# Kernel tuning notes

Measured on AMD Instinct MI355X. Metric: run time of the kernel, lower is better.

Reference implementation:

```python
import jax, jax.numpy as jnp
import numpy as np

M_TOKENS, D_IN, D_OUT = 4096, 4096, 16384


def setup_inputs() -> dict:
    key = jax.random.key(0)
    k1, k2, k3, k4 = jax.random.split(key, 4)
    x = jax.random.normal(k1, (M_TOKENS, D_IN), dtype=jnp.float32)
    # pre-quantized int8 weight, stored [K, N] as in qweight_kn
    qweight_kn = jax.random.randint(k2, (D_IN, D_OUT), -127, 128, dtype=jnp.int8)
    # per-output-channel weight dequant scales (float16 buffer, used as fp32 in kernel)
    weight_scales = jax.random.uniform(k3, (D_OUT,), dtype=jnp.float32, minval=1e-3, maxval=2e-2)
    bias = jax.random.normal(k4, (D_OUT,), dtype=jnp.float32) * 0.01
    return {"x": x, "qweight_kn": qweight_kn, "weight_scales": weight_scales, "bias": bias}


def reference(x, qweight_kn, weight_scales, bias):
    target_dtype = x.dtype
    x2 = x.reshape(-1, x.shape[-1])  # [M, K]
    # dynamic per-token (per-row) symmetric quantization
    x_max = jnp.max(jnp.abs(x2), axis=-1, keepdims=True).astype(jnp.float32) + 1e-5
    x_scales = x_max / 127.0  # [M, 1]
    x_int8 = jnp.clip(jnp.round(x2.astype(jnp.float32) / x_scales), -128, 127).astype(jnp.int8)
    acc = jax.lax.dot_general(
        x_int8, qweight_kn,
        dimension_numbers=(((1,), (0,)), ((), ())),
        preferred_element_type=jnp.int32,
    )  # [M, N] int32
    # fused dequant: row act-scale * col weight-scale, plus bias
    c = acc.astype(jnp.float32) * x_scales * weight_scales[None, :].astype(jnp.float32)
    c = c + bias[None, :]
    out = c.astype(jnp.bfloat16)  # kernel stores bf16
    return out.reshape(*x.shape[:-1], -1).astype(target_dtype)
```

## Files before the change

### kernel.cpp

```cpp
#include <hip/hip_runtime.h>
#include <hip/hip_bf16.h>
#include <stdint.h>

typedef int v4i __attribute__((ext_vector_type(4)));

#define GM 4096
#define GN 16384
#define GK 4096
#define BM 256
#define BN 256
#define BK 64
#define NT (GK / BK)

__device__ __forceinline__ void gload16(const void* g, void* l) {
  __builtin_amdgcn_global_load_lds(
      (const __attribute__((address_space(1))) void*)g,
      (__attribute__((address_space(3))) void*)l, 16, 0, 0);
}

__global__ __launch_bounds__(256) void quant_rows(
    const float* __restrict__ x, int8_t* __restrict__ xq2,
    float* __restrict__ xs, int K) {
  const int row = blockIdx.x;
  const int t = threadIdx.x;
  const float4* src = (const float4*)(x + (size_t)row * K) + t * 4;
  float4 v[4];
  float m = 0.f;
#pragma unroll
  for (int i = 0; i < 4; ++i) {
    v[i] = src[i];
    m = fmaxf(m, fmaxf(fmaxf(fabsf(v[i].x), fabsf(v[i].y)),
                       fmaxf(fabsf(v[i].z), fabsf(v[i].w))));
  }
#pragma unroll
  for (int off = 1; off < 64; off <<= 1)
    m = fmaxf(m, __shfl_xor(m, off, 64));
  __shared__ float wmax[4];
  if ((t & 63) == 0) wmax[t >> 6] = m;
  __syncthreads();
  const float gm = fmaxf(fmaxf(wmax[0], wmax[1]), fmaxf(wmax[2], wmax[3]));
  const float scale = (gm + 1e-5f) / 127.0f;
  if (t == 0) xs[row] = scale;
  unsigned packed[4];
#pragma unroll
  for (int i = 0; i < 4; ++i) {
    float fv[4] = {v[i].x, v[i].y, v[i].z, v[i].w};
    unsigned p = 0;
#pragma unroll
    for (int j = 0; j < 4; ++j) {
      int q = (int)rintf(fv[j] / scale);
      q = max(-128, min(127, q));
      p |= (unsigned)(q & 0xff) << (8 * j);
    }
    packed[i] = p;
  }
  const int tm = row >> 8, f = (row >> 4) & 15, fr = row & 15;
  const int kt = t >> 2, kg = t & 3;
  int8_t* dst =
      xq2 + ((((size_t)(tm * 64 + kt) * 16 + f) * 64) + fr + 16 * kg) * 16;
  *(int4*)dst =
      make_int4((int)packed[0], (int)packed[1], (int)packed[2], (int)packed[3]);
}

__global__ __launch_bounds__(256) void transpose_pack(
    const int* __restrict__ W32, int8_t* __restrict__ Wt2, int K, int N) {
  const int t = threadIdx.x;
  const int tn = blockIdx.x;
  const int kt = blockIdx.y;
  const int nq = t & 63;
  const int kg = t >> 6;
  const int n0 = tn * 256 + nq * 4;
  const int kb = kt * 64 + kg * 16;

  v4i r[16];
#pragma unroll
  for (int k = 0; k < 16; ++k)
    r[k] = *(const v4i*)(W32 + (size_t)(kb + k) * N + n0);

  int o[4][4];
#pragma unroll
  for (int i = 0; i < 4; ++i)
#pragma unroll
    for (int j = 0; j < 4; ++j)
      o[i][j] = (r[4 * j + 0][i] & 0xff) | ((r[4 * j + 1][i] & 0xff) << 8) |
                ((r[4 * j + 2][i] & 0xff) << 16) | (r[4 * j + 3][i] << 24);

  int8_t* base = Wt2 + (((size_t)(tn * 64 + kt) * 16 + (nq >> 2)) * 64 +
                        4 * (nq & 3) + 16 * kg) * 16;
#pragma unroll
  for (int i = 0; i < 4; ++i)
    *(v4i*)(base + i * 16) = *(v4i*)&o[i][0];
}

__global__ __launch_bounds__(512, 2) void gemm_i8(
    const int8_t* __restrict__ Xq2, const int8_t* __restrict__ Wt2,
    const float* __restrict__ xs, const float* __restrict__ wsc,
    const float* __restrict__ bias, float* __restrict__ C) {
  __shared__ __align__(16) int8_t lA[4][16384];

  const int t = threadIdx.x;
  const int lane = t & 63;
  const int w = t >> 6;
  const int wr = w >> 2;
  const int wc = w & 3;
  const int fr = lane & 15;
  const int kg = lane >> 4;

  const int bid = blockIdx.x;
  const int xcd = bid & 7;
  const int q = bid >> 3;
  const int tm = q & 15;
  const int tn = xcd * 8 + (q >> 4);
  const size_t rowA0 = (size_t)tm * BM;
  const size_t rowB0 = (size_t)tn * BN;

  const int8_t* aqB = Xq2 + (size_t)tm * 1048576 + w * 2048 + (size_t)lane * 16;
  const int dstO = w * 2048;

#define STAGE(KT, SLOT)                                           \
  {                                                               \
    const int8_t* p = aqB + (size_t)(KT)*16384;                   \
    gload16(p, &lA[(SLOT)][0] + dstO);                            \
    gload16(p + 1024, &lA[(SLOT)][0] + dstO + 1024);              \
  }

  const int8_t* bq = Wt2 + (size_t)tn * 1048576 + wc * 4096 + (size_t)lane * 16;

  v4i acc[8][4] = {};
  v4i areg[8], breg[4][4];

#define LD(dst, ptr)                                        \
  asm volatile("global_load_dwordx4 %0, %1, off"            \
               : "=v"(dst)                                  \
               : "v"(ptr)                                   \
               : "memory")

#define LOADB(KT, S)                                        \
  {                                                         \
    const int8_t* bp = bq + (size_t)(KT)*16384;             \
    LD(breg[S][0], bp);                                     \
    LD(breg[S][1], bp + 1024);                              \
    LD(breg[S][2], bp + 2048);                              \
    LD(breg[S][3], bp + 3072);                              \
  }

#define RD_A(MI, SLOT)                                                     \
  areg[MI] = *(const v4i*)&lA[(SLOT)][(wr * 8 + (MI)) * 1024 + lane * 16];

#define SB __builtin_amdgcn_sched_barrier(0)

#define BODY(T, SLOT)                                                         \
  {                                                                           \
    asm volatile("s_waitcnt vmcnt(12)" ::: "memory");                         \
    __builtin_amdgcn_s_barrier();  \
    SB;                                                                       \
    STAGE(((T) + 3) & (NT - 1), ((SLOT) + 3) & 3);                            \
    LOADB(((T) + 3) & (NT - 1), ((SLOT) + 3) & 3);                            \
    SB;                                                                       \
    RD_A(0, SLOT); RD_A(1, SLOT); RD_A(2, SLOT); RD_A(3, SLOT);               \
    SB;                                                                       \
    RD_A(4, SLOT); RD_A(5, SLOT); RD_A(6, SLOT); RD_A(7, SLOT);               \
    SB;                                                                       \
    asm volatile("s_waitcnt lgkmcnt(4)" ::: "memory");        \
    SB;                                                                       \
    __builtin_amdgcn_s_setprio(1);                                            \
    _Pragma("unroll") for (int mi = 0; mi < 4; ++mi)                          \
        _Pragma("unroll") for (int nj = 0; nj < 4; ++nj)                      \
            acc[mi][nj] = __builtin_amdgcn_mfma_i32_16x16x64_i8(              \
                areg[mi], breg[SLOT][nj], acc[mi][nj], 0, 0, 0);              \
    __builtin_amdgcn_s_setprio(0);                                            \
    asm volatile("s_waitcnt lgkmcnt(0)" ::: "memory");        \
    SB;                                                                       \
    __builtin_amdgcn_s_setprio(1);                                            \
    _Pragma("unroll") for (int mi = 4; mi < 8; ++mi)                          \
        _Pragma("unroll") for (int nj = 0; nj < 4; ++nj)                      \
            acc[mi][nj] = __builtin_amdgcn_mfma_i32_16x16x64_i8(              \
                areg[mi], breg[SLOT][nj], acc[mi][nj], 0, 0, 0);              \
    __builtin_amdgcn_s_setprio(0);                                            \
  }

  STAGE(0, 0);
  LOADB(0, 0);
  STAGE(1, 1);
  LOADB(1, 1);
  STAGE(2, 2);
  LOADB(2, 2);

  for (int kt = 0; kt < NT; kt += 4) {
    BODY(kt, 0);
    BODY(kt + 1, 1);
    BODY(kt + 2, 2);
    BODY(kt + 3, 3);
  }
  asm volatile("s_waitcnt vmcnt(0) lgkmcnt(0)" ::: "memory");
  SB;

#pragma unroll
  for (int nj = 0; nj < 4; ++nj) {
    const int col_l = wc * 64 + nj * 16 + fr;
    const float wsv = wsc[rowB0 + col_l];
    const float bv = bias[rowB0 + col_l];
#pragma unroll
    for (int mi = 0; mi < 8; ++mi) {
#pragma unroll
      for (int r = 0; r < 4; ++r) {
        const size_t row = rowA0 + wr * 128 + mi * 16 + kg * 4 + r;
        const float f = (float)acc[mi][nj][r] * xs[row] * wsv + bv;
        C[row * GN + rowB0 + col_l] = __bfloat162float(__float2bfloat16(f));
      }
    }
  }
}

extern "C" void kernel_launch(void* const* d_in, const int* in_sizes, int n_in,
                              void* d_out, int out_size, void* d_ws, size_t ws_size,
                              hipStream_t stream) {
  const int M = GM, K = GK, N = GN;
  const float* x = (const float*)d_in[0];
  const int* W32 = (const int*)d_in[1];
  const float* wsc = (const float*)d_in[2];
  const float* bias = (const float*)d_in[3];
  float* out = (float*)d_out;

  float* xs = (float*)d_ws;
  int8_t* Xq2 = (int8_t*)d_ws + 16384;
  int8_t* Wt2 = (int8_t*)d_ws + 16384 + (size_t)M * K;

  transpose_pack<<<dim3(N / 256, K / 64), 256, 0, stream>>>(W32, Wt2, K, N);
  quant_rows<<<M, 256, 0, stream>>>(x, Xq2, xs, K);
  gemm_i8<<<dim3((M / BM) * (N / BN)), 512, 0, stream>>>(Xq2, Wt2, xs, wsc, bias,
                                                         out);
}
```

Measured before the change: 422.2 us.

## Restructure GEMM main loop into double-buffered LDS and register pipeline

```diff
diff --git a/kernel.cpp b/kernel.cpp
--- a/kernel.cpp
+++ b/kernel.cpp
@@ -96,7 +96,7 @@
     const int8_t* __restrict__ Xq2, const int8_t* __restrict__ Wt2,
     const float* __restrict__ xs, const float* __restrict__ wsc,
     const float* __restrict__ bias, float* __restrict__ C) {
-  __shared__ __align__(16) int8_t lA[4][16384];
+  __shared__ __align__(16) int8_t lA[2][16384];
 
   const int t = threadIdx.x;
   const int lane = t & 63;
@@ -127,7 +127,7 @@
   const int8_t* bq = Wt2 + (size_t)tn * 1048576 + wc * 4096 + (size_t)lane * 16;
 
   v4i acc[8][4] = {};
-  v4i areg[8], breg[4][4];
+  v4i areg[2][8], breg[2][4];
 
 #define LD(dst, ptr)                                        \
   asm volatile("global_load_dwordx4 %0, %1, off"            \
@@ -144,56 +144,56 @@
     LD(breg[S][3], bp + 3072);                              \
   }
 
-#define RD_A(MI, SLOT)                                                     \
-  areg[MI] = *(const v4i*)&lA[(SLOT)][(wr * 8 + (MI)) * 1024 + lane * 16];
+#define RD_A8(P)                                                            \
+  _Pragma("unroll") for (int mi = 0; mi < 8; ++mi) areg[P][mi] =            \
+      *(const v4i*)&lA[(P)][(wr * 8 + mi) * 1024 + lane * 16];
+
+#define MFMA_ALL(PB)                                                        \
+  __builtin_amdgcn_s_setprio(1);                                            \
+  _Pragma("unroll") for (int mi = 0; mi < 8; ++mi)                          \
+      _Pragma("unroll") for (int nj = 0; nj < 4; ++nj)                      \
+          acc[mi][nj] = __builtin_amdgcn_mfma_i32_16x16x64_i8(              \
+              areg[PB][mi], breg[PB][nj], acc[mi][nj], 0, 0, 0);            \
+  __builtin_amdgcn_s_setprio(0);
 
 #define SB __builtin_amdgcn_sched_barrier(0)
 
-#define BODY(T, SLOT)                                                         \
+#define BODY(T, P)                                                            \
   {                                                                           \
-    asm volatile("s_waitcnt vmcnt(12)" ::: "memory");                         \
-    __builtin_amdgcn_s_barrier();  \
-    SB;                                                                       \
-    STAGE(((T) + 3) & (NT - 1), ((SLOT) + 3) & 3);                            \
-    LOADB(((T) + 3) & (NT - 1), ((SLOT) + 3) & 3);                            \
-    SB;                                                                       \
-    RD_A(0, SLOT); RD_A(1, SLOT); RD_A(2, SLOT); RD_A(3, SLOT);               \
-    SB;                                                                       \
-    RD_A(4, SLOT); RD_A(5, SLOT); RD_A(6, SLOT); RD_A(7, SLOT);               \
-    SB;                                                                       \
-    asm volatile("s_waitcnt lgkmcnt(4)" ::: "memory");        \
-    SB;                                                                       \
-    __builtin_amdgcn_s_setprio(1);                                            \
-    _Pragma("unroll") for (int mi = 0; mi < 4; ++mi)                          \
-        _Pragma("unroll") for (int nj = 0; nj < 4; ++nj)                      \
-            acc[mi][nj] = __builtin_amdgcn_mfma_i32_16x16x64_i8(              \
-                areg[mi], breg[SLOT][nj], acc[mi][nj], 0, 0, 0);              \
-    __builtin_amdgcn_s_setprio(0);                                            \
-    asm volatile("s_waitcnt lgkmcnt(0)" ::: "memory");        \
-    SB;                                                                       \
-    __builtin_amdgcn_s_setprio(1);                                            \
-    _Pragma("unroll") for (int mi = 4; mi < 8; ++mi)                          \
-        _Pragma("unroll") for (int nj = 0; nj < 4; ++nj)                      \
-            acc[mi][nj] = __builtin_amdgcn_mfma_i32_16x16x64_i8(              \
-                areg[mi], breg[SLOT][nj], acc[mi][nj], 0, 0, 0);              \
-    __builtin_amdgcn_s_setprio(0);                                            \
+       \
+      \
+                                  \
+    asm volatile("s_waitcnt vmcnt(4)" ::: "memory");                          \
+    __builtin_amdgcn_s_barrier();                                             \
+    STAGE(((T) + 1) & (NT - 1), ((P) ^ 1));                                   \
+    SB;                                                                       \
+    RD_A8(P);                                                                 \
+    SB;                                                                       \
+    MFMA_ALL((P) ^ 1);      \
+    asm volatile("s_waitcnt lgkmcnt(0)" ::: "memory");   \
+    SB;                                                                       \
+    LOADB(((T) + 1) & (NT - 1), ((P) ^ 1));      \
+    SB;                                                                       \
   }
 
   STAGE(0, 0);
+  STAGE(1, 1);
   LOADB(0, 0);
-  STAGE(1, 1);
   LOADB(1, 1);
-  STAGE(2, 2);
-  LOADB(2, 2);
-
-  for (int kt = 0; kt < NT; kt += 4) {
+  asm volatile("s_waitcnt vmcnt(0)" ::: "memory");
+  __builtin_amdgcn_s_barrier();
+  RD_A8(0);
+  asm volatile("s_waitcnt lgkmcnt(0)" ::: "memory");
+  SB;
+
+  BODY(1, 1);
+  for (int kt = 2; kt < NT; kt += 2) {
     BODY(kt, 0);
     BODY(kt + 1, 1);
-    BODY(kt + 2, 2);
-    BODY(kt + 3, 3);
   }
   asm volatile("s_waitcnt vmcnt(0) lgkmcnt(0)" ::: "memory");
   SB;
+  MFMA_ALL(1);
 
 #pragma unroll
   for (int nj = 0; nj < 4; ++nj) {
```

Result: no change. 416.7 us (-1.3%).

## Shrink GEMM tiles to 128x128 with double-buffered pipeline and higher occupancy

Applied to the files above, without the earlier changes.

```diff
diff --git a/kernel.cpp b/kernel.cpp
--- a/kernel.cpp
+++ b/kernel.cpp
@@ -7,8 +7,8 @@
 #define GM 4096
 #define GN 16384
 #define GK 4096
-#define BM 256
-#define BN 256
+#define BM 128
+#define BN 128
 #define BK 64
 #define NT (GK / BK)
 
@@ -92,11 +92,11 @@
     *(v4i*)(base + i * 16) = *(v4i*)&o[i][0];
 }
 
-__global__ __launch_bounds__(512, 2) void gemm_i8(
+__global__ __launch_bounds__(512, 4) void gemm_i8(
     const int8_t* __restrict__ Xq2, const int8_t* __restrict__ Wt2,
     const float* __restrict__ xs, const float* __restrict__ wsc,
     const float* __restrict__ bias, float* __restrict__ C) {
-  __shared__ __align__(16) int8_t lA[4][16384];
+  __shared__ __align__(16) int8_t lA[2][8192];
 
   const int t = threadIdx.x;
   const int lane = t & 63;
@@ -109,25 +109,18 @@
   const int bid = blockIdx.x;
   const int xcd = bid & 7;
   const int q = bid >> 3;
-  const int tm = q & 15;
-  const int tn = xcd * 8 + (q >> 4);
+  const int tm = q & 31;
+  const int tn = xcd * 16 + (q >> 5);
   const size_t rowA0 = (size_t)tm * BM;
   const size_t rowB0 = (size_t)tn * BN;
 
-  const int8_t* aqB = Xq2 + (size_t)tm * 1048576 + w * 2048 + (size_t)lane * 16;
-  const int dstO = w * 2048;
-
-#define STAGE(KT, SLOT)                                           \
-  {                                                               \
-    const int8_t* p = aqB + (size_t)(KT)*16384;                   \
-    gload16(p, &lA[(SLOT)][0] + dstO);                            \
-    gload16(p + 1024, &lA[(SLOT)][0] + dstO + 1024);              \
-  }
-
-  const int8_t* bq = Wt2 + (size_t)tn * 1048576 + wc * 4096 + (size_t)lane * 16;
-
-  v4i acc[8][4] = {};
-  v4i areg[8], breg[4][4];
+  const int8_t* aq = Xq2 + (size_t)(tm >> 1) * 1048576 +
+                     ((tm & 1) * 8 + w) * 1024 + (size_t)lane * 16;
+  const int8_t* bq = Wt2 + (size_t)(tn >> 1) * 1048576 +
+                     ((tn & 1) * 8 + wc * 2) * 1024 + (size_t)lane * 16;
+
+  v4i acc[4][2] = {};
+  v4i areg[4], breg[2][2];
 
 #define LD(dst, ptr)                                        \
   asm volatile("global_load_dwordx4 %0, %1, off"            \
@@ -135,76 +128,67 @@
                : "v"(ptr)                                   \
                : "memory")
 
+#define STAGE(KT, S) gload16(aq + (size_t)(KT)*16384, &lA[(S)][0] + w * 1024);
 #define LOADB(KT, S)                                        \
   {                                                         \
     const int8_t* bp = bq + (size_t)(KT)*16384;             \
     LD(breg[S][0], bp);                                     \
     LD(breg[S][1], bp + 1024);                              \
-    LD(breg[S][2], bp + 2048);                              \
-    LD(breg[S][3], bp + 3072);                              \
-  }
-
-#define RD_A(MI, SLOT)                                                     \
-  areg[MI] = *(const v4i*)&lA[(SLOT)][(wr * 8 + (MI)) * 1024 + lane * 16];
+  }
+
+#define RD_A(MI, S)                                                        \
+  areg[MI] = *(const v4i*)&lA[(S)][(wr * 4 + (MI)) * 1024 + lane * 16];
 
 #define SB __builtin_amdgcn_sched_barrier(0)
 
-#define BODY(T, SLOT)                                                         \
+#define BODY(T, P)                                                            \
   {                                                                           \
-    asm volatile("s_waitcnt vmcnt(12)" ::: "memory");                         \
-    __builtin_amdgcn_s_barrier();  \
-    SB;                                                                       \
-    STAGE(((T) + 3) & (NT - 1), ((SLOT) + 3) & 3);                            \
-    LOADB(((T) + 3) & (NT - 1), ((SLOT) + 3) & 3);                            \
-    SB;                                                                       \
-    RD_A(0, SLOT); RD_A(1, SLOT); RD_A(2, SLOT); RD_A(3, SLOT);               \
-    SB;                                                                       \
-    RD_A(4, SLOT); RD_A(5, SLOT); RD_A(6, SLOT); RD_A(7, SLOT);               \
-    SB;                                                                       \
-    asm volatile("s_waitcnt lgkmcnt(4)" ::: "memory");        \
+            \
+    asm volatile("s_waitcnt vmcnt(0)" ::: "memory");                          \
+    __builtin_amdgcn_s_barrier();    \
+    STAGE(((T) + 1) & (NT - 1), (P) ^ 1);                                     \
+    LOADB(((T) + 1) & (NT - 1), (P) ^ 1);                                     \
+    SB;                                                                       \
+    RD_A(0, P); RD_A(1, P); RD_A(2, P); RD_A(3, P);                           \
+    SB;                                                                       \
+    asm volatile("s_waitcnt lgkmcnt(2)" ::: "memory");       \
     SB;                                                                       \
     __builtin_amdgcn_s_setprio(1);                                            \
-    _Pragma("unroll") for (int mi = 0; mi < 4; ++mi)                          \
-        _Pragma("unroll") for (int nj = 0; nj < 4; ++nj)                      \
+    _Pragma("unroll") for (int mi = 0; mi < 2; ++mi)                          \
+        _Pragma("unroll") for (int nj = 0; nj < 2; ++nj)                      \
             acc[mi][nj] = __builtin_amdgcn_mfma_i32_16x16x64_i8(              \
-                areg[mi], breg[SLOT][nj], acc[mi][nj], 0, 0, 0);              \
+                areg[mi], breg[P][nj], acc[mi][nj], 0, 0, 0);                 \
     __builtin_amdgcn_s_setprio(0);                                            \
-    asm volatile("s_waitcnt lgkmcnt(0)" ::: "memory");        \
+    asm volatile("s_waitcnt lgkmcnt(0)" ::: "memory");       \
     SB;                                                                       \
     __builtin_amdgcn_s_setprio(1);                                            \
-    _Pragma("unroll") for (int mi = 4; mi < 8; ++mi)                          \
-        _Pragma("unroll") for (int nj = 0; nj < 4; ++nj)                      \
+    _Pragma("unroll") for (int mi = 2; mi < 4; ++mi)                          \
+        _Pragma("unroll") for (int nj = 0; nj < 2; ++nj)                      \
             acc[mi][nj] = __builtin_amdgcn_mfma_i32_16x16x64_i8(              \
-                areg[mi], breg[SLOT][nj], acc[mi][nj], 0, 0, 0);              \
+                areg[mi], breg[P][nj], acc[mi][nj], 0, 0, 0);                 \
     __builtin_amdgcn_s_setprio(0);                                            \
   }
 
   STAGE(0, 0);
   LOADB(0, 0);
-  STAGE(1, 1);
-  LOADB(1, 1);
-  STAGE(2, 2);
-  LOADB(2, 2);
-
-  for (int kt = 0; kt < NT; kt += 4) {
+
+  for (int kt = 0; kt < NT; kt += 2) {
     BODY(kt, 0);
     BODY(kt + 1, 1);
-    BODY(kt + 2, 2);
-    BODY(kt + 3, 3);
   }
   asm volatile("s_waitcnt vmcnt(0) lgkmcnt(0)" ::: "memory");
   SB;
 
 #pragma unroll
-  for (int nj = 0; nj < 4; ++nj) {
-    const int col_l = wc * 64 + nj * 16 + fr;
+  for (int nj = 0; nj < 2; ++nj) {
+    const int col_l = wc * 32 + nj * 16 + fr;
     const float wsv = wsc[rowB0 + col_l];
     const float bv = bias[rowB0 + col_l];
 #pragma unroll
-    for (int mi = 0; mi < 8; ++mi) {
+    for (int mi = 0; mi < 4; ++mi) {
 #pragma unroll
       for (int r = 0; r < 4; ++r) {
-        const size_t row = rowA0 + wr * 128 + mi * 16 + kg * 4 + r;
+        const size_t row = rowA0 + wr * 64 + mi * 16 + kg * 4 + r;
         const float f = (float)acc[mi][nj][r] * xs[row] * wsv + bv;
         C[row * GN + rowB0 + col_l] = __bfloat162float(__float2bfloat16(f));
       }
```

Measured after the change: 604.1 us. 43.1% more time.
